# Optimization experiments

Hardware: AMD Instinct MI355X
Metric: run time of the kernel (lower is better)

Reference implementation:

```python
import jax, jax.numpy as jnp
import numpy as np

TEMPERATURE = 1.0
PRED_PER_IM = 100
INVALID = np.arange(60, 80)  # invalid class logit indices (constant)


def setup_inputs() -> dict:
    key = jax.random.key(0)
    k1, k2, k3, k4, k5 = jax.random.split(key, 5)
    B, Q, C = 256, 1000, 81
    return {
        "pred_logits": jax.random.normal(k1, (B, Q, C), jnp.float32),
        "pred_obj": jax.random.normal(k2, (B, Q), jnp.float32),
        "pred_boxes": jax.random.uniform(k3, (B, Q, 4), jnp.float32),  # cxcywh in [0,1)
        "pred_unk": jax.random.normal(k4, (B, Q), jnp.float32),
        "target_sizes": jax.random.uniform(k5, (B, 2), jnp.float32, minval=480.0, maxval=1333.0),  # (h, w)
    }


def _postprocess(pred_logits, pred_obj, pred_boxes, pred_unk, target_sizes):
    B, Q, C = pred_logits.shape
    # mask invalid classes with a huge negative logit
    logits = pred_logits.at[:, :, INVALID].set(-1e11)
    obj_prob = jnp.exp(-TEMPERATURE * pred_obj)[..., None]            # [B,Q,1]
    prob = obj_prob * jax.nn.sigmoid(logits)                          # [B,Q,C]
    prob = prob.at[:, :, INVALID].set(0.0)
    unk = jax.nn.sigmoid(pred_unk)                                    # [B,Q]
    prob = prob * (1.0 - unk[..., None])
    prob = prob.at[:, :, -1].set(obj_prob[..., 0] * unk)              # unknown class slot
    # flattened top-k over (query, class)
    scores, idx = jax.lax.top_k(prob.reshape(B, Q * C), PRED_PER_IM)  # [B,K]
    topk_boxes = idx // C
    labels = idx % C
    # cxcywh -> xyxy
    cx, cy, w, h = jnp.split(pred_boxes, 4, axis=-1)
    xyxy = jnp.concatenate([cx - 0.5 * w, cy - 0.5 * h, cx + 0.5 * w, cy + 0.5 * h], axis=-1)
    boxes = jnp.take_along_axis(xyxy, topk_boxes[..., None], axis=1)  # [B,K,4]
    img_h, img_w = target_sizes[:, 0], target_sizes[:, 1]
    scale = jnp.stack([img_w, img_h, img_w, img_h], axis=1)           # [B,4]
    boxes = boxes * scale[:, None, :]
    return scores, labels, boxes


def reference(pred_logits, pred_obj, pred_boxes, pred_unk, target_sizes):
    return _postprocess(pred_logits, pred_obj, pred_boxes, pred_unk, target_sizes)
```

## Files before the change

kernel.cpp:

```cpp
#include <hip/hip_runtime.h>
#include <math.h>

#define BATCH  256
#define NQ     1000
#define NC     81
#define QC     81000
#define CHUNKS (QC / 4)
#define TOPK   100
#define NBINS  4096
#define CAP    4096
#define CAP2   1024
#define NT     1024

__device__ __forceinline__ float sigmoidf(float x) {
    if (x >= 0.f) return 1.f / (1.f + expf(-x));
    float e = expf(x);
    return e / (1.f + e);
}

__device__ __forceinline__ float fast_sig(float x) {
    return __builtin_amdgcn_rcpf(1.f + __expf(-x));
}

struct Smem {
    float    P[NQ];
    float    Pm2[NQ];
    float    op[NQ];
    float    omun[NQ];
    float    last[NQ];
    unsigned hist[NBINS];
    float    cv[CAP];
    int      ci[CAP];
    float    cv2[CAP2];
    int      ci2[CAP2];
    unsigned cnt;
    unsigned cnt2;
    unsigned thr;
};

__device__ unsigned scan_threshold(Smem& s, int tid) {
    __syncthreads();
    if (tid < 64) {
        unsigned c = 0;
        #pragma unroll
        for (int j = 0; j < 64; j += 4) {
            uint4 h = *(const uint4*)&s.hist[tid * 64 + j];
            c += h.x + h.y + h.z + h.w;
        }
        unsigned ssum = c;
        #pragma unroll
        for (int off = 1; off < 64; off <<= 1) {
            unsigned o = __shfl_down(ssum, off, 64);
            if (tid + off < 64) ssum += o;
        }
        unsigned long long bal = __ballot(ssum >= TOPK);
        int cb = 63 - __clzll(bal);
        unsigned tb = 0;
        if (cb >= 0) {
            unsigned S_cb = __shfl(ssum, cb, 64);
            unsigned c_cb = __shfl(c, cb, 64);
            unsigned acc  = S_cb - c_cb;
            unsigned f  = s.hist[cb * 64 + tid];
            unsigned fs = f;
            #pragma unroll
            for (int off = 1; off < 64; off <<= 1) {
                unsigned o = __shfl_down(fs, off, 64);
                if (tid + off < 64) fs += o;
            }
            unsigned long long bal2 = __ballot(acc + fs >= TOPK);
            int fb = 63 - __clzll(bal2);
            tb = (unsigned)(cb * 64 + fb);
        }
        if (tid == 0) s.thr = tb;
    }
    __syncthreads();
    return s.thr;
}

__device__ __forceinline__ void do_chunk(Smem& s, const float4& v4, int q, int c,
                                         unsigned thbits, bool do_hist) {
    float xs[4] = {v4.x, v4.y, v4.z, v4.w};
    #pragma unroll
    for (int k = 0; k < 4; ++k) {
        int ck = c + k, qk = q;
        if (ck >= NC) { ck -= NC; ++qk; }
        if (ck < 60) {
            float v = s.P[qk] * fast_sig(xs[k]);
            unsigned u = __float_as_uint(v);
            if (u >= thbits) {
                if (do_hist) atomicAdd(&s.hist[u >> 19], 1u);
                float pv = (s.op[qk] * sigmoidf(xs[k])) * s.omun[qk];
                unsigned p = atomicAdd(&s.cnt, 1u);
                if (p < CAP) { s.cv[p] = pv; s.ci[p] = qk * NC + ck; }
            }
        }
    }
}

__device__ void scan_chunks(Smem& s, const float4* lg4, unsigned thbits,
                            bool do_hist, int tid) {
    int e = 4 * tid;
    int q = e / NC;
    int c = e - q * NC;
    for (int i4 = tid; i4 < CHUNKS; i4 += 2 * NT) {
        int qb = q + 50, cb = c + 46;
        if (cb >= NC) { cb -= NC; ++qb; }
        bool hasB = (i4 + NT) < CHUNKS;

        float4 va, vb;
        bool da = false, db = false;
        if (__float_as_uint(s.Pm2[q]) >= thbits) { va = lg4[i4]; da = true; }
        if (hasB && __float_as_uint(s.Pm2[qb]) >= thbits) { vb = lg4[i4 + NT]; db = true; }
        if (da) do_chunk(s, va, q, c, thbits, do_hist);
        if (db) do_chunk(s, vb, qb, cb, thbits, do_hist);

        c += 11; q += 101;
        if (c >= NC) { c -= NC; ++q; }
    }
}

__device__ void collect80(Smem& s, unsigned thbits, int tid) {
    for (int q = tid; q < NQ; q += NT) {
        float v = s.last[q];
        if (__float_as_uint(v) >= thbits) {
            unsigned p = atomicAdd(&s.cnt, 1u);
            if (p < CAP) { s.cv[p] = v; s.ci[p] = q * NC + 80; }
        }
    }
}

__global__ __launch_bounds__(NT) void postprocess_kernel(
    const float* __restrict__ logits,
    const float* __restrict__ obj,
    const float* __restrict__ boxes,
    const float* __restrict__ unk,
    const float* __restrict__ tsz,
    float* __restrict__ out)
{
    __shared__ Smem s;
    const int b   = blockIdx.x;
    const int tid = threadIdx.x;
    const float4* lg4 = (const float4*)(logits + (size_t)b * QC);

    for (int i = tid; i < NBINS; i += NT) s.hist[i] = 0;
    if (tid == 0) { s.cnt = 0; s.cnt2 = 0; }
    for (int q = tid; q < NQ; q += NT) {
        float op = expf(-obj[b * NQ + q]);
        float un = sigmoidf(unk[b * NQ + q]);
        float om = 1.f - un;
        s.op[q] = op; s.omun[q] = om; s.P[q] = op * om; s.last[q] = op * un;
    }
    __syncthreads();

    for (int q = tid; q < NQ; q += NT) {
        float pm = s.P[q];
        if (q + 1 < NQ) pm = fmaxf(pm, s.P[q + 1]);
        s.Pm2[q] = pm;
        atomicAdd(&s.hist[__float_as_uint(s.last[q]) >> 19], 1u);
    }

    unsigned t0  = scan_threshold(s, tid);
    unsigned th0 = (t0 >= 2 ? t0 - 2 : 0) << 19;

    scan_chunks(s, lg4, th0, true, tid);
    collect80(s, th0, tid);
    __syncthreads();

    unsigned tF = scan_threshold(s, tid);

    if (s.cnt > CAP) {
        unsigned thF = (tF >= 2 ? tF - 2 : 0) << 19;
        __syncthreads();
        if (tid == 0) s.cnt = 0;
        __syncthreads();
        scan_chunks(s, lg4, thF, false, tid);
        collect80(s, thF, tid);
        __syncthreads();
    }

    const int n = (int)min(s.cnt, (unsigned)CAP);

    const float vF = __uint_as_float(((tF >= 1) ? tF - 1 : 0) << 19);
    for (int i = tid; i < n; i += NT) {
        float v = s.cv[i];
        if (v >= vF) {
            unsigned p = atomicAdd(&s.cnt2, 1u);
            if (p < CAP2) { s.cv2[p] = v; s.ci2[p] = s.ci[i]; }
        }
    }
    __syncthreads();

    const float* rv; const int* ri; int m;
    if (s.cnt2 <= CAP2) { rv = s.cv2; ri = s.ci2; m = (int)s.cnt2; }
    else                { rv = s.cv;  ri = s.ci;  m = n; }

    const float* bx = boxes + (size_t)b * NQ * 4;
    const float img_h = tsz[b * 2 + 0];
    const float img_w = tsz[b * 2 + 1];
    float* o_sc = out + (size_t)b * TOPK;
    float* o_lb = out + (size_t)BATCH * TOPK + (size_t)b * TOPK;
    float* o_bx = out + (size_t)2 * BATCH * TOPK + (size_t)b * TOPK * 4;

    for (int i = tid; i < m; i += NT) {
        float vi = rv[i];
        int   ei = ri[i];
        int r = 0;
        for (int j = 0; j < m; ++j) {
            float vj = rv[j];
            int   ej = ri[j];
            r += (vj > vi) || (vj == vi && ej < ei);
        }
        if (r < TOPK) {
            o_sc[r] = vi;
            o_lb[r] = (float)(ei % NC);
            int q = ei / NC;
            float cx = bx[q * 4 + 0];
            float cy = bx[q * 4 + 1];
            float w  = bx[q * 4 + 2];
            float h  = bx[q * 4 + 3];
            o_bx[r * 4 + 0] = (cx - 0.5f * w) * img_w;
            o_bx[r * 4 + 1] = (cy - 0.5f * h) * img_h;
            o_bx[r * 4 + 2] = (cx + 0.5f * w) * img_w;
            o_bx[r * 4 + 3] = (cy + 0.5f * h) * img_h;
        }
    }
}

extern "C" void kernel_launch(void* const* d_in, const int* in_sizes, int n_in,
                              void* d_out, int out_size, void* d_ws, size_t ws_size,
                              hipStream_t stream) {
    const float* pred_logits = (const float*)d_in[0];
    const float* pred_obj    = (const float*)d_in[1];
    const float* pred_boxes  = (const float*)d_in[2];
    const float* pred_unk    = (const float*)d_in[3];
    const float* target_sz   = (const float*)d_in[4];
    float* out = (float*)d_out;
    postprocess_kernel<<<BATCH, NT, 0, stream>>>(
        pred_logits, pred_obj, pred_boxes, pred_unk, target_sz, out);
}
```

Before: 155.9 us.

## Split logits scan into histogram pass and tight-threshold collect pass

Replaces the single scan, which both histogrammed and collected candidates, with a histogram-only pass followed by a second full pass that collects only at the refined threshold. This removes the second filtering stage and its extra buffers. Candidates are packed into uint2 entries, and the ranking compares them as unsigned bit patterns. The scan loop now issues four float4 loads per iteration for more memory-level parallelism, and shared memory use shrinks. The cost is always reading the logits twice (subject to the per-query gating) instead of usually once, in exchange for a smaller candidate set and less shared-memory pressure.

```diff
diff --git a/kernel.cpp b/kernel.cpp
--- a/kernel.cpp
+++ b/kernel.cpp
@@ -8,8 +8,7 @@
 #define CHUNKS (QC / 4)
 #define TOPK   100
 #define NBINS  4096
-#define CAP    4096
-#define CAP2   1024
+#define CAP    2048
 #define NT     1024
 
 __device__ __forceinline__ float sigmoidf(float x) {
@@ -29,12 +28,8 @@
     float    omun[NQ];
     float    last[NQ];
     unsigned hist[NBINS];
-    float    cv[CAP];
-    int      ci[CAP];
-    float    cv2[CAP2];
-    int      ci2[CAP2];
+    uint2    cand[CAP];
     unsigned cnt;
-    unsigned cnt2;
     unsigned thr;
 };
 
@@ -60,8 +55,7 @@
             unsigned S_cb = __shfl(ssum, cb, 64);
             unsigned c_cb = __shfl(c, cb, 64);
             unsigned acc  = S_cb - c_cb;
-            unsigned f  = s.hist[cb * 64 + tid];
-            unsigned fs = f;
+            unsigned fs = s.hist[cb * 64 + tid];
             #pragma unroll
             for (int off = 1; off < 64; off <<= 1) {
                 unsigned o = __shfl_down(fs, off, 64);
@@ -77,54 +71,69 @@
     return s.thr;
 }
 
-__device__ __forceinline__ void do_chunk(Smem& s, const float4& v4, int q, int c,
-                                         unsigned thbits, bool do_hist) {
+__device__ __forceinline__ void chunk_hist(Smem& s, const float4& v4, int q, int c,
+                                           unsigned thbits) {
     float xs[4] = {v4.x, v4.y, v4.z, v4.w};
     #pragma unroll
     for (int k = 0; k < 4; ++k) {
         int ck = c + k, qk = q;
         if (ck >= NC) { ck -= NC; ++qk; }
         if (ck < 60) {
-            float v = s.P[qk] * fast_sig(xs[k]);
-            unsigned u = __float_as_uint(v);
+            unsigned u = __float_as_uint(s.P[qk] * fast_sig(xs[k]));
+            if (u >= thbits) atomicAdd(&s.hist[u >> 19], 1u);
+        }
+    }
+}
+
+__device__ __forceinline__ void chunk_collect(Smem& s, const float4& v4, int q, int c,
+                                              unsigned thbits) {
+    float xs[4] = {v4.x, v4.y, v4.z, v4.w};
+    #pragma unroll
+    for (int k = 0; k < 4; ++k) {
+        int ck = c + k, qk = q;
+        if (ck >= NC) { ck -= NC; ++qk; }
+        if (ck < 60) {
+            unsigned u = __float_as_uint(s.P[qk] * fast_sig(xs[k]));
             if (u >= thbits) {
-                if (do_hist) atomicAdd(&s.hist[u >> 19], 1u);
                 float pv = (s.op[qk] * sigmoidf(xs[k])) * s.omun[qk];
                 unsigned p = atomicAdd(&s.cnt, 1u);
-                if (p < CAP) { s.cv[p] = pv; s.ci[p] = qk * NC + ck; }
+                if (p < CAP)
+                    s.cand[p] = make_uint2(__float_as_uint(pv), (unsigned)(qk * NC + ck));
             }
         }
     }
 }
 
-__device__ void scan_chunks(Smem& s, const float4* lg4, unsigned thbits,
-                            bool do_hist, int tid) {
-    int e = 4 * tid;
-    int q = e / NC;
-    int c = e - q * NC;
-    for (int i4 = tid; i4 < CHUNKS; i4 += 2 * NT) {
-        int qb = q + 50, cb = c + 46;
-        if (cb >= NC) { cb -= NC; ++qb; }
-        bool hasB = (i4 + NT) < CHUNKS;
-
-        float4 va, vb;
-        bool da = false, db = false;
-        if (__float_as_uint(s.Pm2[q]) >= thbits) { va = lg4[i4]; da = true; }
-        if (hasB && __float_as_uint(s.Pm2[qb]) >= thbits) { vb = lg4[i4 + NT]; db = true; }
-        if (da) do_chunk(s, va, q, c, thbits, do_hist);
-        if (db) do_chunk(s, vb, qb, cb, thbits, do_hist);
-
-        c += 11; q += 101;
-        if (c >= NC) { c -= NC; ++q; }
+template <bool COLLECT>
+__device__ void scan(Smem& s, const float4* __restrict__ lg4, unsigned thbits, int tid) {
+    int q = (4 * tid) / NC;
+    int c = 4 * tid - q * NC;
+    for (int base = tid; base < CHUNKS; base += 4 * NT) {
+        float4 vv[4]; bool dd[4]; int qs[4], cs[4];
+        int qq = q, cc = c;
+        #pragma unroll
+        for (int t = 0; t < 4; ++t) {
+            int i4 = base + t * NT;
+            qs[t] = qq; cs[t] = cc;
+            dd[t] = (i4 < CHUNKS) && (__float_as_uint(s.Pm2[qq]) >= thbits);
+            if (dd[t]) vv[t] = lg4[i4];
+            cc += 46; qq += 50; if (cc >= NC) { cc -= NC; ++qq; }
+        }
+        #pragma unroll
+        for (int t = 0; t < 4; ++t) if (dd[t]) {
+            if (COLLECT) chunk_collect(s, vv[t], qs[t], cs[t], thbits);
+            else         chunk_hist   (s, vv[t], qs[t], cs[t], thbits);
+        }
+        c += 22; q += 202; if (c >= NC) { c -= NC; ++q; }
     }
 }
 
 __device__ void collect80(Smem& s, unsigned thbits, int tid) {
     for (int q = tid; q < NQ; q += NT) {
-        float v = s.last[q];
-        if (__float_as_uint(v) >= thbits) {
+        unsigned u = __float_as_uint(s.last[q]);
+        if (u >= thbits) {
             unsigned p = atomicAdd(&s.cnt, 1u);
-            if (p < CAP) { s.cv[p] = v; s.ci[p] = q * NC + 80; }
+            if (p < CAP) s.cand[p] = make_uint2(u, (unsigned)(q * NC + 80));
         }
     }
 }
@@ -142,8 +151,11 @@
     const int tid = threadIdx.x;
     const float4* lg4 = (const float4*)(logits + (size_t)b * QC);
 
-    for (int i = tid; i < NBINS; i += NT) s.hist[i] = 0;
-    if (tid == 0) { s.cnt = 0; s.cnt2 = 0; }
+    {
+        int i = tid * 4;
+        *(uint4*)&s.hist[i] = make_uint4(0u, 0u, 0u, 0u);
+    }
+    if (tid == 0) s.cnt = 0;
     for (int q = tid; q < NQ; q += NT) {
         float op = expf(-obj[b * NQ + q]);
         float un = sigmoidf(unk[b * NQ + q]);
@@ -159,40 +171,27 @@
         atomicAdd(&s.hist[__float_as_uint(s.last[q]) >> 19], 1u);
     }
 
-    unsigned t0  = scan_threshold(s, tid);
-    unsigned th0 = (t0 >= 2 ? t0 - 2 : 0) << 19;
-
-    scan_chunks(s, lg4, th0, true, tid);
-    collect80(s, th0, tid);
-    __syncthreads();
+    unsigned t0 = scan_threshold(s, tid);
+
+    scan<false>(s, lg4, t0 << 19, tid);
 
     unsigned tF = scan_threshold(s, tid);
 
+    unsigned thC = ((tF >= 1) ? tF - 1 : 0) << 19;
+    scan<true>(s, lg4, thC, tid);
+    collect80(s, thC, tid);
+    __syncthreads();
+
     if (s.cnt > CAP) {
-        unsigned thF = (tF >= 2 ? tF - 2 : 0) << 19;
         __syncthreads();
         if (tid == 0) s.cnt = 0;
         __syncthreads();
-        scan_chunks(s, lg4, thF, false, tid);
-        collect80(s, thF, tid);
+        scan<true>(s, lg4, tF << 19, tid);
+        collect80(s, tF << 19, tid);
         __syncthreads();
     }
 
-    const int n = (int)min(s.cnt, (unsigned)CAP);
-
-    const float vF = __uint_as_float(((tF >= 1) ? tF - 1 : 0) << 19);
-    for (int i = tid; i < n; i += NT) {
-        float v = s.cv[i];
-        if (v >= vF) {
-            unsigned p = atomicAdd(&s.cnt2, 1u);
-            if (p < CAP2) { s.cv2[p] = v; s.ci2[p] = s.ci[i]; }
-        }
-    }
-    __syncthreads();
-
-    const float* rv; const int* ri; int m;
-    if (s.cnt2 <= CAP2) { rv = s.cv2; ri = s.ci2; m = (int)s.cnt2; }
-    else                { rv = s.cv;  ri = s.ci;  m = n; }
+    const int m = (int)min(s.cnt, (unsigned)CAP);
 
     const float* bx = boxes + (size_t)b * NQ * 4;
     const float img_h = tsz[b * 2 + 0];
@@ -202,16 +201,15 @@
     float* o_bx = out + (size_t)2 * BATCH * TOPK + (size_t)b * TOPK * 4;
 
     for (int i = tid; i < m; i += NT) {
-        float vi = rv[i];
-        int   ei = ri[i];
+        uint2 ci = s.cand[i];
         int r = 0;
         for (int j = 0; j < m; ++j) {
-            float vj = rv[j];
-            int   ej = ri[j];
-            r += (vj > vi) || (vj == vi && ej < ei);
+            uint2 cj = s.cand[j];
+            r += (cj.x > ci.x) || (cj.x == ci.x && cj.y < ci.y);
         }
         if (r < TOPK) {
-            o_sc[r] = vi;
+            int ei = (int)ci.y;
+            o_sc[r] = __uint_as_float(ci.x);
             o_lb[r] = (float)(ei % NC);
             int q = ei / NC;
             float cx = bx[q * 4 + 0];
```

Result: faster. 145.3 us (-6.8%).
